# Optimization experiments

Measured on AMD Instinct MI355X. Metric: run time of the kernel, lower is better.

Reference implementation:

```python
import jax, jax.numpy as jnp
import numpy as np

LSH_NUM_PROJS = 7
BLOCK_SIZE = 256      # key block size
SAMPLE_SIZE = 256
B, H, N, D = 1, 32, 8192, 128


def _gray_perm(num_projs):
    # AngularLSH._unit_hamming_distance_array: Gray-code bucket permutation
    a = np.array([0, 1], dtype=np.int32)
    for _ in range(num_projs - 1):
        a = np.concatenate([a, np.flip(a) + a.shape[0]])
    return jnp.asarray(a)


def _lsh_hash(x, proj_dir, perm):
    # x: [B,H,N,D], proj_dir: [D,R] -> bucket ids [B,H,N]
    bits = jnp.einsum('bhnd,dr->bhnr', x, proj_dir) > 0
    enc = 2 ** jnp.arange(proj_dir.shape[-1], dtype=jnp.int32)
    bin_ids = jnp.sum(bits.astype(jnp.int32) * enc, axis=-1)
    return perm[bin_ids]


def _attn_lse(q, k, v, scale, bias=None):
    # exact attention returning output and log-sum-exp of scaled scores
    s = jnp.einsum('...qd,...kd->...qk', q, k) * scale
    if bias is not None:
        s = s + bias
    m = jnp.max(s, axis=-1, keepdims=True)
    p = jnp.exp(s - m)
    denom = jnp.sum(p, axis=-1, keepdims=True)
    attn = jnp.einsum('...qk,...kd->...qd', p, v) / denom
    lse = m + jnp.log(denom)  # [..., q, 1]
    return attn, lse


def _take(x, idx):
    # gather along the sequence axis (dim 2); idx: [B,H,M]
    return jnp.take_along_axis(x, idx[..., None], axis=2)


def hyper_attention(q, k, v, proj_dir, sampled_set):
    b, h, n, d = q.shape
    scale = d ** -0.5
    perm = _gray_perm(LSH_NUM_PROJS)
    # 1) sortLSH: sort q and k by angular-LSH bucket (stable)
    q_idx = jnp.argsort(_lsh_hash(q, proj_dir, perm), axis=2)
    k_idx = jnp.argsort(_lsh_hash(k, proj_dir, perm), axis=2)
    q_idx_inv = jnp.argsort(q_idx, axis=2)
    q_s = _take(q, q_idx)
    k_s = _take(k, k_idx)
    v_s = _take(v, k_idx)
    nb = n // BLOCK_SIZE          # number of key blocks
    qbs = n // nb                 # query block size
    # block-diagonal exact attention in sorted order
    qb = q_s.reshape(b, h, nb, qbs, d)
    kb = k_s.reshape(b, h, nb, BLOCK_SIZE, d)
    vb = v_s.reshape(b, h, nb, BLOCK_SIZE, d)
    attn_blk, lse_blk = _attn_lse(qb, kb, vb, scale)
    attn_blk = attn_blk.reshape(b, h, n, d)
    lse_blk = lse_blk.reshape(b, h, n, 1)
    attn_blk = _take(attn_blk, q_idx_inv)
    lse_blk = _take(lse_blk, q_idx_inv)
    # 2) residual: uniform sampling of keys (indices into sorted key order)
    s_size = sampled_set.shape[-1]
    k_sub = _take(k_s, sampled_set)   # [B,H,S,D]
    v_sub = _take(v_s, sampled_set)
    # mask out samples falling in the query's own diagonal block
    same_block = (jnp.arange(n)[None, None, :, None] // qbs) == (sampled_set[:, :, None, :] // BLOCK_SIZE)
    bias = jnp.where(same_block, jnp.finfo(q.dtype).min, 0.0).astype(q.dtype)
    attn_res, lse_res = _attn_lse(q_s, k_sub, v_sub, scale, bias=bias)
    lse_res = lse_res + jnp.log(n / s_size)  # importance weight n_key/sample_size
    attn_res = _take(attn_res, q_idx_inv)
    lse_res = _take(lse_res, q_idx_inv)
    # 3) combine estimators: softmax-weighted average in log space
    lse = jnp.logaddexp(lse_blk, lse_res)
    return jnp.exp(lse_blk - lse) * attn_blk + jnp.exp(lse_res - lse) * attn_res


def setup_inputs() -> dict:
    key = jax.random.key(0)
    k1, k2, k3, k4, k5 = jax.random.split(key, 5)
    return {
        'queries': jax.random.normal(k1, (B, H, N, D), dtype=jnp.float32),
        'keys': jax.random.normal(k2, (B, H, N, D), dtype=jnp.float32),
        'vals': jax.random.normal(k3, (B, H, N, D), dtype=jnp.float32),
        'proj_dir': jax.random.normal(k4, (D, LSH_NUM_PROJS), dtype=jnp.float32),
        'sampled_set': jax.random.randint(k5, (B, H, SAMPLE_SIZE), 0, N),
    }


def reference(queries, keys, vals, proj_dir, sampled_set):
    return hyper_attention(queries, keys, vals, proj_dir, sampled_set)
```

## Files before the change

kernel.cpp:

```cpp
#include <hip/hip_runtime.h>
#include <hip/hip_bf16.h>
#include <math.h>

#define Hh 32
#define Nseq 8192
#define Dh 128
#define NBd 32
#define BLKSZ 256
#define SAMP 256
#define CHK 64
#define NCH 8
#define LOG32 3.4657359027997265f
#define SCALE 0.088388347648318447f
#define SKW 136
#define SVW 72

typedef float f32x4 __attribute__((ext_vector_type(4)));
typedef unsigned ui32x4 __attribute__((ext_vector_type(4)));
typedef __bf16 bf16x8 __attribute__((ext_vector_type(8)));

__device__ __forceinline__ f32x4 mfma16(bf16x8 a, bf16x8 b, f32x4 c) {
  return __builtin_amdgcn_mfma_f32_16x16x32_bf16(a, b, c, 0, 0, 0);
}

__device__ __forceinline__ bf16x8 cvt8(const float* __restrict__ p) {
  float4 a = ((const float4*)p)[0];
  float4 b = ((const float4*)p)[1];
  bf16x8 r;
  r[0] = (__bf16)a.x; r[1] = (__bf16)a.y; r[2] = (__bf16)a.z; r[3] = (__bf16)a.w;
  r[4] = (__bf16)b.x; r[5] = (__bf16)b.y; r[6] = (__bf16)b.z; r[7] = (__bf16)b.w;
  return r;
}

__device__ __forceinline__ bf16x8 cvt8v(float4 a, float4 b) {
  bf16x8 r;
  r[0] = (__bf16)a.x; r[1] = (__bf16)a.y; r[2] = (__bf16)a.z; r[3] = (__bf16)a.w;
  r[4] = (__bf16)b.x; r[5] = (__bf16)b.y; r[6] = (__bf16)b.z; r[7] = (__bf16)b.w;
  return r;
}

__device__ __forceinline__ unsigned pack2(float a, float b, float& ra, float& rb) {
  __bf16 ba = (__bf16)a, bb = (__bf16)b;
  ra = (float)ba; rb = (float)bb;
  return ((unsigned)__builtin_bit_cast(unsigned short, bb) << 16) |
         (unsigned)__builtin_bit_cast(unsigned short, ba);
}

__global__ __launch_bounds__(256) void lsh_hash_kernel(
    const float* __restrict__ q, const float* __restrict__ k,
    const float* __restrict__ proj, int* __restrict__ buckets) {
  int row = blockIdx.x * 256 + threadIdx.x;
  const float* x = ((row >> 18) ? k : q) + (size_t)(row & (Hh * Nseq - 1)) * Dh;
  double acc[7] = {0, 0, 0, 0, 0, 0, 0};
#pragma unroll 8
  for (int d0 = 0; d0 < Dh; d0 += 4) {
    float4 xv = *(const float4*)(x + d0);
    double x0 = (double)xv.x, x1 = (double)xv.y, x2 = (double)xv.z, x3 = (double)xv.w;
#pragma unroll
    for (int j = 0; j < 7; j++) {
      acc[j] = fma(x0, (double)proj[(d0 + 0) * 7 + j], acc[j]);
      acc[j] = fma(x1, (double)proj[(d0 + 1) * 7 + j], acc[j]);
      acc[j] = fma(x2, (double)proj[(d0 + 2) * 7 + j], acc[j]);
      acc[j] = fma(x3, (double)proj[(d0 + 3) * 7 + j], acc[j]);
    }
  }
  int bin = 0;
#pragma unroll
  for (int j = 0; j < 7; j++) bin |= (acc[j] > 0.0 ? 1 : 0) << j;
  buckets[row] = bin ^ (bin >> 1);
}

__global__ __launch_bounds__(64) void bucket_sort_kernel(
    const int* __restrict__ buckets, int* __restrict__ idx) {
  __shared__ unsigned hist[64][128];
  int t = threadIdx.x;
  int base = blockIdx.x * Nseq;
  for (int b = 0; b < 128; b++) hist[t][b] = 0;
  __syncthreads();
  for (int i = 0; i < 128; i++) {
    int b = buckets[base + t * 128 + i];
    hist[t][b]++;
  }
  __syncthreads();
  int b0 = 2 * t, b1 = 2 * t + 1;
  unsigned tot0 = 0, tot1 = 0;
  for (int tt = 0; tt < 64; tt++) { unsigned h = hist[tt][b0]; hist[tt][b0] = tot0; tot0 += h; }
  for (int tt = 0; tt < 64; tt++) { unsigned h = hist[tt][b1]; hist[tt][b1] = tot1; tot1 += h; }
  unsigned pair = tot0 + tot1;
  unsigned scan = pair;
  for (int s = 1; s < 64; s <<= 1) {
    unsigned u = __shfl_up(scan, s);
    if (t >= s) scan += u;
  }
  unsigned start0 = scan - pair;
  unsigned start1 = start0 + tot0;
  __syncthreads();
  for (int tt = 0; tt < 64; tt++) { hist[tt][b0] += start0; hist[tt][b1] += start1; }
  __syncthreads();
  for (int i = 0; i < 128; i++) {
    int gi = t * 128 + i;
    int b = buckets[base + gi];
    unsigned pos = hist[t][b]++;
    idx[base + pos] = gi;
  }
}

__global__ __launch_bounds__(256) void permute_samp_kernel(
    const float* __restrict__ k, const float* __restrict__ v,
    const int* __restrict__ k_idx, const int* __restrict__ sampled,
    __bf16* __restrict__ K_sp, __bf16* __restrict__ V_sp) {
  __shared__ __attribute__((aligned(16))) __bf16 s_t[Dh][SVW];
  const int tile = blockIdx.x, bh = blockIdx.y;
  const int t = threadIdx.x;
  const int j = t >> 2, seg = (t & 3) * 32;
  const int dpos = tile * 64 + j;
  const int sp = sampled[bh * SAMP + dpos];
  const int orig = k_idx[bh * Nseq + sp];
  {
    const float4* kp = (const float4*)(k + ((size_t)bh * Nseq + orig) * Dh + seg);
    __bf16* dst = K_sp + ((size_t)bh * SAMP + dpos) * Dh + seg;
#pragma unroll
    for (int i = 0; i < 4; i++) *(bf16x8*)(dst + i * 8) = cvt8v(kp[2 * i], kp[2 * i + 1]);
  }
  {
    const float4* vp = (const float4*)(v + ((size_t)bh * Nseq + orig) * Dh + seg);
#pragma unroll
    for (int i = 0; i < 8; i++) {
      float4 a = vp[i];
      s_t[seg + i * 4 + 0][j] = (__bf16)a.x;
      s_t[seg + i * 4 + 1][j] = (__bf16)a.y;
      s_t[seg + i * 4 + 2][j] = (__bf16)a.z;
      s_t[seg + i * 4 + 3][j] = (__bf16)a.w;
    }
  }
  __syncthreads();
  {
    int d = t >> 1, half = (t & 1) * 32;
    __bf16* dst = V_sp + ((size_t)(bh * Dh + d)) * SAMP + tile * 64 + half;
    const __bf16* srcp = &s_t[d][half];
#pragma unroll
    for (int i = 0; i < 4; i++) *(ui32x4*)(dst + i * 8) = *(const ui32x4*)(srcp + i * 8);
  }
}

__global__ __launch_bounds__(512, 2) void hyper_attn_kernel(
    const float* __restrict__ q, const float* __restrict__ k, const float* __restrict__ v,
    const __bf16* __restrict__ K_sp, const __bf16* __restrict__ V_sp,
    const int* __restrict__ sampled, const int* __restrict__ q_idx,
    const int* __restrict__ k_idx, float* __restrict__ out) {
  __shared__ int s_orig[BLKSZ];
  __shared__ __attribute__((aligned(16))) float s_add[SAMP];
  __shared__ __attribute__((aligned(16))) __bf16 s_k[2][CHK][SKW];
  __shared__ __attribute__((aligned(16))) __bf16 s_vt[2][Dh][SVW];

  const int c = blockIdx.x, bh = blockIdx.y;
  const int tid = threadIdx.x;
  const int w = tid >> 6, l = tid & 63;
  const int l4 = l >> 4, lm = l & 15;
  const int jk = tid >> 3, pk = tid & 7;
  const int dv = tid >> 2, ks = (tid & 3) * 16;

  {
    int jj = tid;
    if (jj < BLKSZ) {
      s_orig[jj] = k_idx[bh * Nseq + c * BLKSZ + jj];
    } else {
      int sp = sampled[bh * SAMP + (jj - BLKSZ)];
      s_add[jj - BLKSZ] = ((sp >> 8) == c) ? -1e38f : LOG32;
    }
  }

  bf16x8 qf[2][4];
  const int* qi = q_idx + bh * Nseq + c * BLKSZ + w * 32;
#pragma unroll
  for (int rt = 0; rt < 2; rt++) {
    int orig = qi[rt * 16 + lm];
    const float* qp = q + ((size_t)bh * Nseq + orig) * Dh + l4 * 8;
#pragma unroll
    for (int dc = 0; dc < 4; dc++) qf[rt][dc] = cvt8(qp + dc * 32);
  }

  f32x4 O[2][8];
  float mrow[2] = {-INFINITY, -INFINITY};
  float lsum[2] = {0.f, 0.f};
#pragma unroll
  for (int rt = 0; rt < 2; rt++)
#pragma unroll
    for (int dt = 0; dt < 8; dt++) { O[rt][dt][0]=0.f; O[rt][dt][1]=0.f; O[rt][dt][2]=0.f; O[rt][dt][3]=0.f; }

  __syncthreads();

  {
    int origk = s_orig[jk];
    const float* kp = k + ((size_t)bh * Nseq + origk) * Dh + pk * 16;
    *(bf16x8*)&s_k[0][jk][pk * 16]     = cvt8(kp);
    *(bf16x8*)&s_k[0][jk][pk * 16 + 8] = cvt8(kp + 8);
    int origv = s_orig[l];
    const float* vp = v + ((size_t)bh * Nseq + origv) * Dh + w * 16;
    float4 A = ((const float4*)vp)[0], B = ((const float4*)vp)[1];
    float4 C = ((const float4*)vp)[2], Dv = ((const float4*)vp)[3];
    float tmp[16] = {A.x,A.y,A.z,A.w,B.x,B.y,B.z,B.w,C.x,C.y,C.z,C.w,Dv.x,Dv.y,Dv.z,Dv.w};
#pragma unroll
    for (int dd = 0; dd < 16; dd++) s_vt[0][w * 16 + dd][l] = (__bf16)tmp[dd];
  }
  __syncthreads();

  const int laneA = lm + 32 * (l4 & 1);
  const bool hi = (l4 >> 1) & 1;

  for (int ch = 0; ch < NCH; ch++) {
    const int cur = ch & 1;
    const int cn = ch + 1;
    const bool pfg = (cn < 4);
    const bool pfc = (cn >= 4 && cn < NCH);

    float4 kA, kB, kC, kD, vA, vB, vC, vD;
    ui32x4 ksA, ksB, vsA, vsB;
    if (pfg) {
      int origk = s_orig[cn * CHK + jk];
      const float4* kp = (const float4*)(k + ((size_t)bh * Nseq + origk) * Dh + pk * 16);
      kA = kp[0]; kB = kp[1]; kC = kp[2]; kD = kp[3];
      int origv = s_orig[cn * CHK + l];
      const float4* vp = (const float4*)(v + ((size_t)bh * Nseq + origv) * Dh + w * 16);
      vA = vp[0]; vB = vp[1]; vC = vp[2]; vD = vp[3];
    } else if (pfc) {
      const __bf16* kp = K_sp + ((size_t)(bh * SAMP + (cn - 4) * CHK + jk)) * Dh + pk * 16;
      ksA = *(const ui32x4*)kp; ksB = *(const ui32x4*)(kp + 8);
      const __bf16* vp = V_sp + ((size_t)(bh * Dh + dv)) * SAMP + (cn - 4) * CHK + ks;
      vsA = *(const ui32x4*)vp; vsB = *(const ui32x4*)(vp + 8);
    }

    float sc[2][4][4];
#pragma unroll
    for (int ct = 0; ct < 4; ct++) {
      f32x4 acc0, acc1;
      acc0[0]=0.f;acc0[1]=0.f;acc0[2]=0.f;acc0[3]=0.f;
      acc1[0]=0.f;acc1[1]=0.f;acc1[2]=0.f;acc1[3]=0.f;
#pragma unroll
      for (int dc = 0; dc < 4; dc++) {
        bf16x8 kf = *(const bf16x8*)&s_k[cur][ct * 16 + lm][dc * 32 + l4 * 8];
        acc0 = mfma16(kf, qf[0][dc], acc0);
        acc1 = mfma16(kf, qf[1][dc], acc1);
      }
      f32x4 addv;
      if (ch < 4) { addv[0]=0.f; addv[1]=0.f; addv[2]=0.f; addv[3]=0.f; }
      else addv = *(const f32x4*)&s_add[(ch - 4) * CHK + ct * 16 + l4 * 4];
#pragma unroll
      for (int r = 0; r < 4; r++) {
        sc[0][ct][r] = acc0[r] * SCALE + addv[r];
        sc[1][ct][r] = acc1[r] * SCALE + addv[r];
      }
    }

    unsigned q01[2][4], q23[2][4];
#pragma unroll
    for (int rt = 0; rt < 2; rt++) {
      float mc = sc[rt][0][0];
#pragma unroll
      for (int ct = 0; ct < 4; ct++)
#pragma unroll
        for (int r = 0; r < 4; r++) mc = fmaxf(mc, sc[rt][ct][r]);
      mc = fmaxf(mc, __shfl_xor(mc, 16));
      mc = fmaxf(mc, __shfl_xor(mc, 32));
      float mn = fmaxf(mrow[rt], mc);
      float alpha = __expf(mrow[rt] - mn);
      mrow[rt] = mn;
      f32x4 aO;
#pragma unroll
      for (int r = 0; r < 4; r++) aO[r] = __shfl(alpha, l4 * 4 + r);
#pragma unroll
      for (int dt = 0; dt < 8; dt++) O[rt][dt] *= aO;
      float rsum = 0.f;
#pragma unroll
      for (int ct = 0; ct < 4; ct++) {
        float p0 = __expf(sc[rt][ct][0] - mn);
        float p1 = __expf(sc[rt][ct][1] - mn);
        float p2 = __expf(sc[rt][ct][2] - mn);
        float p3 = __expf(sc[rt][ct][3] - mn);
        float ra, rb, rc, rd;
        q01[rt][ct] = pack2(p0, p1, ra, rb);
        q23[rt][ct] = pack2(p2, p3, rc, rd);
        rsum += (ra + rb) + (rc + rd);
      }
      rsum += __shfl_xor(rsum, 16);
      rsum += __shfl_xor(rsum, 32);
      lsum[rt] = lsum[rt] * alpha + rsum;
    }

    if (pfg) {
      *(bf16x8*)&s_k[cur ^ 1][jk][pk * 16]     = cvt8v(kA, kB);
      *(bf16x8*)&s_k[cur ^ 1][jk][pk * 16 + 8] = cvt8v(kC, kD);
      float ta[16] = {vA.x,vA.y,vA.z,vA.w,vB.x,vB.y,vB.z,vB.w,
                      vC.x,vC.y,vC.z,vC.w,vD.x,vD.y,vD.z,vD.w};
#pragma unroll
      for (int dd = 0; dd < 16; dd++) s_vt[cur ^ 1][w * 16 + dd][l] = (__bf16)ta[dd];
    } else if (pfc) {
      *(ui32x4*)&s_k[cur ^ 1][jk][pk * 16]     = ksA;
      *(ui32x4*)&s_k[cur ^ 1][jk][pk * 16 + 8] = ksB;
      *(ui32x4*)&s_vt[cur ^ 1][dv][ks]     = vsA;
      *(ui32x4*)&s_vt[cur ^ 1][dv][ks + 8] = vsB;
    }

#pragma unroll
    for (int kc = 0; kc < 2; kc++) {
      bf16x8 pa[2];
#pragma unroll
      for (int rt = 0; rt < 2; rt++) {
        unsigned a0 = __shfl((int)q01[rt][2 * kc],     laneA);
        unsigned b0 = __shfl((int)q01[rt][2 * kc + 1], laneA);
        unsigned a1 = __shfl((int)q23[rt][2 * kc],     laneA);
        unsigned b1 = __shfl((int)q23[rt][2 * kc + 1], laneA);
        unsigned a2 = __shfl((int)q01[rt][2 * kc],     laneA + 16);
        unsigned b2 = __shfl((int)q01[rt][2 * kc + 1], laneA + 16);
        unsigned a3 = __shfl((int)q23[rt][2 * kc],     laneA + 16);
        unsigned b3 = __shfl((int)q23[rt][2 * kc + 1], laneA + 16);
        ui32x4 pw;
        pw[0] = hi ? b0 : a0;
        pw[1] = hi ? b1 : a1;
        pw[2] = hi ? b2 : a2;
        pw[3] = hi ? b3 : a3;
        pa[rt] = __builtin_bit_cast(bf16x8, pw);
      }
#pragma unroll
      for (int dt = 0; dt < 8; dt++) {
        bf16x8 vb = *(const bf16x8*)&s_vt[cur][dt * 16 + lm][kc * 32 + l4 * 8];
        O[0][dt] = mfma16(pa[0], vb, O[0][dt]);
        O[1][dt] = mfma16(pa[1], vb, O[1][dt]);
      }
    }
    __syncthreads();
  }

#pragma unroll
  for (int rt = 0; rt < 2; rt++) {
    float inv = 1.0f / lsum[rt];
    f32x4 invr;
#pragma unroll
    for (int r = 0; r < 4; r++) invr[r] = __shfl(inv, l4 * 4 + r);
#pragma unroll
    for (int r = 0; r < 4; r++) {
      int orow = q_idx[bh * Nseq + c * BLKSZ + w * 32 + rt * 16 + l4 * 4 + r];
      float* op = out + ((size_t)bh * Nseq + orow) * Dh + lm;
#pragma unroll
      for (int dt = 0; dt < 8; dt++) op[dt * 16] = O[rt][dt][r] * invr[r];
    }
  }
}

extern "C" void kernel_launch(void* const* d_in, const int* in_sizes, int n_in,
                              void* d_out, int out_size, void* d_ws, size_t ws_size,
                              hipStream_t stream) {
  const float* q    = (const float*)d_in[0];
  const float* k    = (const float*)d_in[1];
  const float* v    = (const float*)d_in[2];
  const float* proj = (const float*)d_in[3];
  const int* samp   = (const int*)d_in[4];
  float* out = (float*)d_out;

  int* buckets = (int*)d_ws;
  int* idx = buckets + 2 * Hh * Nseq;
  __bf16* K_sp = (__bf16*)(idx + 2 * Hh * Nseq);
  __bf16* V_sp = K_sp + (size_t)Hh * SAMP * Dh;

  lsh_hash_kernel<<<(2 * Hh * Nseq) / 256, 256, 0, stream>>>(q, k, proj, buckets);
  bucket_sort_kernel<<<2 * Hh, 64, 0, stream>>>(buckets, idx);
  permute_samp_kernel<<<dim3(4, Hh), 256, 0, stream>>>(
      k, v, idx + Hh * Nseq , samp, K_sp, V_sp);
  hyper_attn_kernel<<<dim3(NBd, Hh), 512, 0, stream>>>(
      q, k, v, K_sp, V_sp, samp, idx , idx + Hh * Nseq , out);
}
```

Measured before the change: 271.1 us.

## Widen bucket sort to 256 threads and stage attention output through LDS

The counting sort now runs 256 threads per head, each handling 32 keys. It uses 16-bit per-thread histograms, a two-wave prefix scan and register-cached bucket ids, so it no longer reads the buckets from global memory a second time. The attention epilogue writes normalized output tiles into reused shared memory and then stores full 64-byte row segments with vector stores, replacing scattered 4-byte column stores. This adds extra barriers and shared-memory traffic, and the per-thread scan over 256 histogram rows is serial.

```diff
diff --git a/kernel.cpp b/kernel.cpp
--- a/kernel.cpp
+++ b/kernel.cpp
@@ -14,6 +14,7 @@
 #define SCALE 0.088388347648318447f
 #define SKW 136
 #define SVW 72
+#define ORS 132
 
 typedef float f32x4 __attribute__((ext_vector_type(4)));
 typedef unsigned ui32x4 __attribute__((ext_vector_type(4)));
@@ -70,38 +71,69 @@
   buckets[row] = bin ^ (bin >> 1);
 }
 
-__global__ __launch_bounds__(64) void bucket_sort_kernel(
+__global__ __launch_bounds__(256) void bucket_sort_kernel(
     const int* __restrict__ buckets, int* __restrict__ idx) {
-  __shared__ unsigned hist[64][128];
-  int t = threadIdx.x;
-  int base = blockIdx.x * Nseq;
-  for (int b = 0; b < 128; b++) hist[t][b] = 0;
-  __syncthreads();
-  for (int i = 0; i < 128; i++) {
-    int b = buckets[base + t * 128 + i];
+  __shared__ unsigned short hist[256][128];
+  __shared__ unsigned btot[128];
+  __shared__ unsigned wsum[2];
+  const int t = threadIdx.x;
+  const int base = blockIdx.x * Nseq;
+
+  {
+    uint4* h4 = (uint4*)&hist[0][0];
+#pragma unroll
+    for (int j = 0; j < 16; j++) h4[t + j * 256] = uint4{0, 0, 0, 0};
+  }
+  __syncthreads();
+
+  int bloc[32];
+#pragma unroll 8
+  for (int i = 0; i < 32; i++) {
+    int b = buckets[base + t * 32 + i];
+    bloc[i] = b;
     hist[t][b]++;
   }
   __syncthreads();
-  int b0 = 2 * t, b1 = 2 * t + 1;
-  unsigned tot0 = 0, tot1 = 0;
-  for (int tt = 0; tt < 64; tt++) { unsigned h = hist[tt][b0]; hist[tt][b0] = tot0; tot0 += h; }
-  for (int tt = 0; tt < 64; tt++) { unsigned h = hist[tt][b1]; hist[tt][b1] = tot1; tot1 += h; }
-  unsigned pair = tot0 + tot1;
-  unsigned scan = pair;
-  for (int s = 1; s < 64; s <<= 1) {
-    unsigned u = __shfl_up(scan, s);
-    if (t >= s) scan += u;
-  }
-  unsigned start0 = scan - pair;
-  unsigned start1 = start0 + tot0;
-  __syncthreads();
-  for (int tt = 0; tt < 64; tt++) { hist[tt][b0] += start0; hist[tt][b1] += start1; }
-  __syncthreads();
-  for (int i = 0; i < 128; i++) {
-    int gi = t * 128 + i;
-    int b = buckets[base + gi];
+
+  unsigned v = 0;
+  if (t < 128) {
+    unsigned run = 0;
+    for (int cch = 0; cch < 256; cch++) {
+      unsigned h = hist[cch][t];
+      hist[cch][t] = (unsigned short)run;
+      run += h;
+    }
+    btot[t] = run;
+    v = run;
+  }
+  __syncthreads();
+
+  unsigned sc = v;
+  if (t < 128) {
+#pragma unroll
+    for (int s = 1; s < 64; s <<= 1) {
+      unsigned u = __shfl_up(sc, s);
+      if ((t & 63) >= s) sc += u;
+    }
+    if ((t & 63) == 63) wsum[t >> 6] = sc;
+  }
+  __syncthreads();
+  if (t < 128) {
+    unsigned excl = sc - v + ((t >> 6) ? wsum[0] : 0u);
+    btot[t] = excl;
+  }
+  __syncthreads();
+  if (t < 128) {
+    unsigned short e = (unsigned short)btot[t];
+    for (int cch = 0; cch < 256; cch++) hist[cch][t] += e;
+  }
+  __syncthreads();
+
+#pragma unroll 8
+  for (int i = 0; i < 32; i++) {
+    int b = bloc[i];
     unsigned pos = hist[t][b]++;
-    idx[base + pos] = gi;
+    idx[base + pos] = t * 32 + i;
   }
 }
 
@@ -331,18 +363,37 @@
     __syncthreads();
   }
 
+  float invr_[2][4];
 #pragma unroll
   for (int rt = 0; rt < 2; rt++) {
     float inv = 1.0f / lsum[rt];
-    f32x4 invr;
-#pragma unroll
-    for (int r = 0; r < 4; r++) invr[r] = __shfl(inv, l4 * 4 + r);
-#pragma unroll
-    for (int r = 0; r < 4; r++) {
-      int orow = q_idx[bh * Nseq + c * BLKSZ + w * 32 + rt * 16 + l4 * 4 + r];
-      float* op = out + ((size_t)bh * Nseq + orow) * Dh + lm;
-#pragma unroll
-      for (int dt = 0; dt < 8; dt++) op[dt * 16] = O[rt][dt][r] * invr[r];
+#pragma unroll
+    for (int r = 0; r < 4; r++) invr_[rt][r] = __shfl(inv, l4 * 4 + r);
+  }
+  float* lds_o = (float*)s_vt;
+#pragma unroll
+  for (int b = 0; b < 4; b++) {
+    const int rt = b >> 1, pair = b & 1;
+    __syncthreads();
+    if ((l4 >> 1) == pair) {
+      int rbase = (l4 & 1) * 4;
+#pragma unroll
+      for (int r = 0; r < 4; r++) {
+        float* dst = lds_o + (w * 8 + rbase + r) * ORS + lm;
+#pragma unroll
+        for (int dt = 0; dt < 8; dt++) dst[dt * 16] = O[rt][dt][r] * invr_[rt][r];
+      }
+    }
+    __syncthreads();
+    {
+      int rloc = l >> 3, seg = (l & 7) * 16;
+      int g = w * 32 + rt * 16 + pair * 8 + rloc;
+      int orow = q_idx[bh * Nseq + c * BLKSZ + g];
+      const float* src = lds_o + (w * 8 + rloc) * ORS + seg;
+      float* op = out + ((size_t)bh * Nseq + orow) * Dh + seg;
+#pragma unroll
+      for (int i = 0; i < 4; i++)
+        *(f32x4*)(op + i * 4) = *(const f32x4*)(src + i * 4);
     }
   }
 }
@@ -363,7 +414,7 @@
   __bf16* V_sp = K_sp + (size_t)Hh * SAMP * Dh;
 
   lsh_hash_kernel<<<(2 * Hh * Nseq) / 256, 256, 0, stream>>>(q, k, proj, buckets);
-  bucket_sort_kernel<<<2 * Hh, 64, 0, stream>>>(buckets, idx);
+  bucket_sort_kernel<<<2 * Hh, 256, 0, stream>>>(buckets, idx);
   permute_samp_kernel<<<dim3(4, Hh), 256, 0, stream>>>(
       k, v, idx + Hh * Nseq , samp, K_sp, V_sp);
   hyper_attn_kernel<<<dim3(NBd, Hh), 512, 0, stream>>>(
```

Result: slower. 290.9 us (+7.3%).
